# Kernel tuning notes

Measured on AMD Instinct MI355X. Metric: run time of the kernel, lower is better.

## Reference

```python
import jax, jax.numpy as jnp
import numpy as np

B, D, E, H, A = 4096, 1024, 8, 1024, 512  # batch, state_dim, num_options, num_neurons, num_actions


def setup_inputs() -> dict:
    key = jax.random.key(0)
    ks = jax.random.split(key, 16)
    s = 0.02
    return {
        "state": jax.random.normal(ks[0], (B, D), jnp.float32),
        "selected_options": jax.random.randint(ks[1], (B,), 0, E, jnp.int32),
        # option network: Linear(D,H) -> ReLU -> Linear(H,E)
        "Wo1": jax.random.normal(ks[2], (D, H), jnp.float32) * s,
        "bo1": jnp.zeros((H,), jnp.float32),
        "Wo2": jax.random.normal(ks[3], (H, E), jnp.float32) * s,
        "bo2": jnp.zeros((E,), jnp.float32),
        # E expert nets, each: Linear(D,H)+ReLU -> Linear(H,H)+ReLU -> Linear(H,A)
        "We1": jax.random.normal(ks[4], (E, D, H), jnp.float32) * s,
        "be1": jnp.zeros((E, H), jnp.float32),
        "We2": jax.random.normal(ks[5], (E, H, H), jnp.float32) * s,
        "be2": jnp.zeros((E, H), jnp.float32),
        "We3": jax.random.normal(ks[6], (E, H, A), jnp.float32) * s,
        "be3": jnp.zeros((E, A), jnp.float32),
        # termination network: Linear(D,H) -> ReLU -> Linear(H,1) -> Sigmoid
        "Wt1": jax.random.normal(ks[7], (D, H), jnp.float32) * s,
        "bt1": jnp.zeros((H,), jnp.float32),
        "Wt2": jax.random.normal(ks[8], (H, 1), jnp.float32) * s,
        "bt2": jnp.zeros((1,), jnp.float32),
    }


def reference(state, selected_options, Wo1, bo1, Wo2, bo2,
              We1, be1, We2, be2, We3, be3, Wt1, bt1, Wt2, bt2):
    # option head
    option_probs = jax.nn.softmax(jnp.maximum(state @ Wo1 + bo1, 0.0) @ Wo2 + bo2, axis=-1)

    # expert MLPs: compute all experts vectorized, then gather per-sample selected expert.
    # (the torch code loops per sample; equal action sizes so no padding is needed)
    h = jnp.maximum(jnp.einsum("bd,edh->beh", state, We1) + be1, 0.0)   # [B,E,H]
    h = jnp.maximum(jnp.einsum("beh,ehk->bek", h, We2) + be2, 0.0)      # [B,E,H]
    logits = jnp.einsum("beh,eha->bea", h, We3) + be3                   # [B,E,A]
    probs_all = jax.nn.softmax(logits, axis=-1)
    sel = selected_options[:, None, None]
    action_probs = jnp.take_along_axis(probs_all, sel, axis=1)[:, 0, :]  # [B,A]
    selected_actions = jnp.argmax(action_probs, axis=-1)

    # termination head
    termination_prob = jax.nn.sigmoid(jnp.maximum(state @ Wt1 + bt1, 0.0) @ Wt2 + bt2)

    return option_probs, action_probs, termination_prob, selected_options, selected_actions
```

## Files before the change

kernel.cpp:

```cpp
#include <hip/hip_runtime.h>
#include <hip/hip_bf16.h>

#define B_ 4096
#define D_ 1024
#define E_ 8
#define H_ 1024
#define A_ 512
#define PB 6144
#define NTT 24
#define FB_CAP 128
#define FROWS (E_ * FB_CAP)
#define KSPLIT 4
#define MARGIN 3.0e-3f

typedef __attribute__((ext_vector_type(8))) short s16x8;
typedef __attribute__((ext_vector_type(4))) float f32x4;

__device__ __forceinline__ unsigned short f2bf(float f) {
    __hip_bfloat16 h = __float2bfloat16(f);
    return *reinterpret_cast<unsigned short*>(&h);
}
__device__ __forceinline__ float bf2f(unsigned short u) {
    return __uint_as_float(((unsigned int)u) << 16);
}
__device__ __forceinline__ void gload16(const void* g, void* l) {
    __builtin_amdgcn_global_load_lds(
        (const __attribute__((address_space(1))) unsigned int*)g,
        (__attribute__((address_space(3))) unsigned int*)l, 16, 0, 0);
}

__device__ __forceinline__ int a_src_chunk(int lane) { return (((lane & 7) ^ (lane >> 3)) * 8); }

__device__ __forceinline__ int trc(int r, int c) { return (c + r + (r >> 2)) & 63; }

__device__ __forceinline__ void tr_tile_256(const float* __restrict__ src, int Nsrc,
                                            unsigned short* __restrict__ dst, float* T) {
    const int t = threadIdx.x;
    const int c4 = (t & 15) * 4, r0 = t >> 4;
#pragma unroll
    for (int i = 0; i < 8; ++i) {
        const int r = r0 + i * 16;
        const float4 v = *(const float4*)&src[(size_t)r * Nsrc + c4];
        float* Tr = T + r * 64;
        Tr[trc(r, c4 + 0)] = v.x; Tr[trc(r, c4 + 1)] = v.y;
        Tr[trc(r, c4 + 2)] = v.z; Tr[trc(r, c4 + 3)] = v.w;
    }
    __syncthreads();
    const int k4 = (t & 31) * 4, n0 = t >> 5;
#pragma unroll
    for (int i = 0; i < 8; ++i) {
        const int n = n0 + i * 8;
        ushort4 o;
        o.x = f2bf(T[(k4 + 0) * 64 + trc(k4 + 0, n)]);
        o.y = f2bf(T[(k4 + 1) * 64 + trc(k4 + 1, n)]);
        o.z = f2bf(T[(k4 + 2) * 64 + trc(k4 + 2, n)]);
        o.w = f2bf(T[(k4 + 3) * 64 + trc(k4 + 3, n)]);
        *(ushort4*)&dst[(size_t)n * 1024 + k4] = o;
    }
}

__global__ void k_prep(const float* __restrict__ x, unsigned short* __restrict__ y,
                       const float* __restrict__ Wo1, const float* __restrict__ Wt1,
                       unsigned short* __restrict__ Wbf,
                       const float* __restrict__ We1, unsigned short* __restrict__ We1t,
                       const float* __restrict__ We2, unsigned short* __restrict__ We2t,
                       const float* __restrict__ We3, unsigned short* __restrict__ We3t,
                       const int* __restrict__ sel, int* __restrict__ tile_expert,
                       int* __restrict__ rowlist, int* __restrict__ pos_of_row,
                       int* __restrict__ rowlist2, int* __restrict__ cur2) {
    __shared__ float T[128 * 64];
    const int t = threadIdx.x;
    const int bid = blockIdx.x;
    if (bid >= 6401) {
        const int q = bid - 6401;
        const int e = q >> 6, r = q & 63, kt = r >> 3, ntb = r & 7;
        tr_tile_256(We3 + (size_t)e * 524288 + (size_t)(kt * 128) * 512 + ntb * 64, 512,
                    We3t + (size_t)e * 524288 + (size_t)(ntb * 64) * 1024 + kt * 128, T);
        return;
    }
    if (bid >= 5377) {
        const int q = bid - 5377;
        const int e = q >> 7, r = q & 127, kt = r >> 4, ntb = r & 15;
        tr_tile_256(We2 + (size_t)e * 1048576 + (size_t)(kt * 128) * 1024 + ntb * 64, 1024,
                    We2t + (size_t)e * 1048576 + (size_t)(ntb * 64) * 1024 + kt * 128, T);
        return;
    }
    if (bid >= 4353) {
        const int q = bid - 4353;
        const int e = q >> 7, r = q & 127, kt = r >> 4, ntb = r & 15;
        tr_tile_256(We1 + (size_t)e * 1048576 + (size_t)(kt * 128) * 1024 + ntb * 64, 1024,
                    We1t + (size_t)e * 1048576 + (size_t)(ntb * 64) * 1024 + kt * 128, T);
        return;
    }
    if (bid >= 4097) {
        const int q = bid - 4097;
        const int m = q >> 7, r = q & 127, kt = r >> 4, ntb = r & 15;
        const float* src = (m ? Wt1 : Wo1) + (size_t)(kt * 128) * 1024 + ntb * 64;
        tr_tile_256(src, 1024, Wbf + (size_t)(m * 1024 + ntb * 64) * 1024 + kt * 128, T);
        return;
    }
    if (bid > 0) {
        int i = (bid - 1) * 256 + t;
        float4 v = ((const float4*)x)[i];
        ushort4 o;
        o.x = f2bf(v.x); o.y = f2bf(v.y); o.z = f2bf(v.z); o.w = f2bf(v.w);
        ((ushort4*)y)[i] = o;
        return;
    }
    __shared__ int scnt[E_], soff[E_], scur[E_];
    if (t < E_) { scnt[t] = 0; scur[t] = 0; cur2[t] = 0; }
    for (int i = t; i < PB; i += 256) rowlist[i] = -1;
    for (int i = t; i < FROWS; i += 256) rowlist2[i] = -1;
    __syncthreads();
    for (int b = t; b < B_; b += 256) {
        int e = sel[b]; e = e < 0 ? 0 : (e >= E_ ? E_ - 1 : e);
        atomicAdd(&scnt[e], 1);
    }
    __syncthreads();
    if (t == 0) {
        int off = 0;
        for (int e = 0; e < E_; ++e) {
            soff[e] = off;
            int tiles = (scnt[e] + 255) >> 8;
            for (int k = 0; k < tiles; ++k) tile_expert[(off >> 8) + k] = e;
            off += tiles << 8;
        }
        for (int k = off >> 8; k < NTT; ++k) tile_expert[k] = -1;
    }
    __syncthreads();
    for (int b = t; b < B_; b += 256) {
        int e = sel[b]; e = e < 0 ? 0 : (e >= E_ ? E_ - 1 : e);
        int pos = atomicAdd(&scur[e], 1);
        int p = soff[e] + pos; if (p >= PB) p = PB - 1;
        rowlist[p] = b;
        pos_of_row[b] = p;
    }
}

template<int TN>
__device__ __forceinline__ void gemm3(
    const unsigned short* __restrict__ g0, const unsigned short* __restrict__ g1,
    const unsigned short* __restrict__ g2, const unsigned short* __restrict__ g3,
    const unsigned short* __restrict__ Bt, int Kg, const float* __restrict__ bp,
    unsigned short* __restrict__ Cbf, float* __restrict__ Cf, int Ncols, int relu,
    unsigned short* As, unsigned short* Bs)
{
    constexpr int NI = TN / 32;
    constexpr int BTH = TN * 64;
    constexpr int BR = TN / 64;
    const int t = threadIdx.x, lane = t & 63, w = t >> 6;
    const int wr = w >> 1, wc = w & 1;
    const int aseg = w * 2048 + lane * 8;
    const int bseg = w * (BR * 512) + lane * 8;
    const int coffb = a_src_chunk(lane);
    const unsigned short* bsrc = Bt + (size_t)(w * BR * 8 + (lane >> 3)) * Kg + coffb;

    f32x4 acc[4][NI];
#pragma unroll
    for (int i = 0; i < 4; ++i)
#pragma unroll
        for (int j = 0; j < NI; ++j)
#pragma unroll
            for (int r = 0; r < 4; ++r) acc[i][j][r] = 0.f;

#define G_STAGE(IT, BUF) {                                                   \
        const int ko_ = (IT) * 64;                                           \
        const int oa_ = (BUF) * 16384 + aseg;                                \
        gload16(g0 + ko_, As + oa_);                                         \
        gload16(g1 + ko_, As + oa_ + 512);                                   \
        gload16(g2 + ko_, As + oa_ + 1024);                                  \
        gload16(g3 + ko_, As + oa_ + 1536);                                  \
        const int ob_ = (BUF) * BTH + bseg;                                  \
        _Pragma("unroll")                                                    \
        for (int j_ = 0; j_ < BR; ++j_)                                      \
            gload16(bsrc + ko_ + (size_t)(j_ * 8) * Kg, Bs + ob_ + j_ * 512); \
    }

    G_STAGE(0, 0);
    __syncthreads();

    for (int it = 0; it < 16; ++it) {
        const int cb = it & 1;
        if (it + 1 < 16) G_STAGE(it + 1, cb ^ 1);
        __builtin_amdgcn_s_setprio(1);
#pragma unroll
        for (int kq = 0; kq < 2; ++kq) {
            const int sc = kq * 4 + (lane >> 4);
            s16x8 af[4], bfr[NI];
#pragma unroll
            for (int mi = 0; mi < 4; ++mi) {
                const int ar = wr * 64 + mi * 16 + (lane & 15);
                af[mi] = *reinterpret_cast<const s16x8*>(
                    &As[cb * 16384 + ar * 64 + ((sc ^ (ar & 7)) << 3)]);
            }
#pragma unroll
            for (int ni = 0; ni < NI; ++ni) {
                const int br = wc * (TN / 2) + ni * 16 + (lane & 15);
                bfr[ni] = *reinterpret_cast<const s16x8*>(
                    &Bs[cb * BTH + br * 64 + ((sc ^ (br & 7)) << 3)]);
            }
#pragma unroll
            for (int mi = 0; mi < 4; ++mi)
#pragma unroll
                for (int ni = 0; ni < NI; ++ni)
                    acc[mi][ni] = __builtin_amdgcn_mfma_f32_16x16x32_bf16(
                        af[mi], bfr[ni], acc[mi][ni], 0, 0, 0);
        }
        __builtin_amdgcn_s_setprio(0);
        if (it + 1 < 16) __syncthreads();
    }
#undef G_STAGE

    const int cq = lane >> 4, cr = lane & 15;
#pragma unroll
    for (int ni = 0; ni < NI; ++ni) {
        const int col_l = wc * (TN / 2) + ni * 16 + cr;
        const float bv = bp[col_l];
#pragma unroll
        for (int mi = 0; mi < 4; ++mi) {
#pragma unroll
            for (int r = 0; r < 4; ++r) {
                const int row_l = wr * 64 + mi * 16 + cq * 4 + r;
                float v = acc[mi][ni][r] + bv;
                if (relu) v = fmaxf(v, 0.f);
                const size_t idx = (size_t)row_l * Ncols + col_l;
                if (Cbf) Cbf[idx] = f2bf(v);
                if (Cf)  Cf[idx] = v;
            }
        }
    }
}

__global__ __launch_bounds__(512, 2)
void k_d2(const unsigned short* __restrict__ Sbf,
          const int* __restrict__ rowlist, const int* __restrict__ tile_expert,
          const unsigned short* __restrict__ Wbf,
          const float* __restrict__ bo1, const float* __restrict__ bt1,
          const unsigned short* __restrict__ We1t, const float* __restrict__ be1,
          unsigned short* __restrict__ hopt, unsigned short* __restrict__ hterm,
          unsigned short* __restrict__ h1) {
    __shared__ __align__(16) unsigned short SMEM[4 * 16384];
    unsigned short* As = SMEM;
    unsigned short* Bs = SMEM + 2 * 16384;
    const int bid = blockIdx.x;
    const int t = threadIdx.x, lane = t & 63, w = t >> 6;
    const int coff = a_src_chunk(lane);
    const int r0l = w * 32 + (lane >> 3);
    if (bid < 128) {
        const int nt = bid & 7, mt = bid >> 3;
        const unsigned short* g0 = Sbf + (size_t)(mt * 256 + r0l) * D_ + coff;
        const unsigned short* g1 = g0 + (size_t)8 * D_;
        const unsigned short* g2 = g0 + (size_t)16 * D_;
        const unsigned short* g3 = g0 + (size_t)24 * D_;
        int ntRow; const float* bp; unsigned short* C;
        if (nt < 4) { ntRow = nt * 256; bp = bo1 + nt * 256;
                      C = hopt + (size_t)(mt * 256) * H_ + nt * 256; }
        else { ntRow = 1024 + (nt - 4) * 256; bp = bt1 + (nt - 4) * 256;
               C = hterm + (size_t)(mt * 256) * H_ + (nt - 4) * 256; }
        gemm3<256>(g0, g1, g2, g3, Wbf + (size_t)ntRow * 1024, 1024, bp,
                   C, nullptr, H_, 1, As, Bs);
    } else {
        const int q = bid - 128, nt = q & 3, mt = q >> 2;
        const int e = tile_expert[mt]; if (e < 0) return;
        const int base = mt * 256;
        const int sub = rowlist[base]; if (sub < 0) return;
        int r0 = rowlist[base + r0l];      if (r0 < 0) r0 = sub;
        int r1 = rowlist[base + r0l + 8];  if (r1 < 0) r1 = sub;
        int r2 = rowlist[base + r0l + 16]; if (r2 < 0) r2 = sub;
        int r3 = rowlist[base + r0l + 24]; if (r3 < 0) r3 = sub;
        const unsigned short* g0 = Sbf + (size_t)r0 * D_ + coff;
        const unsigned short* g1 = Sbf + (size_t)r1 * D_ + coff;
        const unsigned short* g2 = Sbf + (size_t)r2 * D_ + coff;
        const unsigned short* g3 = Sbf + (size_t)r3 * D_ + coff;
        gemm3<256>(g0, g1, g2, g3,
                   We1t + (size_t)e * 1048576 + (size_t)(nt * 256) * 1024, 1024,
                   be1 + (size_t)e * H_ + nt * 256,
                   h1 + (size_t)(mt * 256) * H_ + nt * 256, nullptr, H_, 1, As, Bs);
    }
}

__global__ __launch_bounds__(512, 2)
void k_d3(const unsigned short* __restrict__ h1, const int* __restrict__ tile_expert,
          const unsigned short* __restrict__ We2t, const float* __restrict__ be2,
          unsigned short* __restrict__ h2) {
    __shared__ __align__(16) unsigned short SMEM[2 * 16384 + 2 * 8192];
    unsigned short* As = SMEM;
    unsigned short* Bs = SMEM + 2 * 16384;
    const int t = threadIdx.x, lane = t & 63, w = t >> 6;
    const int coff = a_src_chunk(lane);
    const int r0l = w * 32 + (lane >> 3);
    const int nt = blockIdx.x & 7, mt = blockIdx.x >> 3;
    const int e = tile_expert[mt]; if (e < 0) return;
    const unsigned short* g0 = h1 + (size_t)(mt * 256 + r0l) * H_ + coff;
    gemm3<128>(g0, g0 + (size_t)8 * H_, g0 + (size_t)16 * H_, g0 + (size_t)24 * H_,
               We2t + (size_t)e * 1048576 + (size_t)(nt * 128) * 1024, 1024,
               be2 + (size_t)e * H_ + nt * 128,
               h2 + (size_t)(mt * 256) * H_ + nt * 128, nullptr, H_, 1, As, Bs);
}

__global__ __launch_bounds__(512, 2)
void k_d5(const unsigned short* __restrict__ h2, const int* __restrict__ tile_expert,
          const unsigned short* __restrict__ We3t, const float* __restrict__ be3,
          float* __restrict__ lgt) {
    __shared__ __align__(16) unsigned short SMEM[2 * 16384 + 2 * 4096];
    unsigned short* As = SMEM;
    unsigned short* Bs = SMEM + 2 * 16384;
    const int t = threadIdx.x, lane = t & 63, w = t >> 6;
    const int coff = a_src_chunk(lane);
    const int r0l = w * 32 + (lane >> 3);
    const int nt = blockIdx.x & 7, mt = blockIdx.x >> 3;
    const int e = tile_expert[mt]; if (e < 0) return;
    const unsigned short* g0 = h2 + (size_t)(mt * 256 + r0l) * H_ + coff;
    gemm3<64>(g0, g0 + (size_t)8 * H_, g0 + (size_t)16 * H_, g0 + (size_t)24 * H_,
              We3t + (size_t)e * 524288 + (size_t)(nt * 64) * 1024, 1024,
              be3 + (size_t)e * A_ + nt * 64,
              nullptr, lgt + (size_t)(mt * 256) * A_ + nt * 64, A_, 0, As, Bs);
}

__device__ __forceinline__ void opt_body(int b, const unsigned short* __restrict__ h,
                                         const float* __restrict__ Wo2, const float* __restrict__ bo2,
                                         float* __restrict__ out, float* sm) {
    const int t = threadIdx.x;
    float acc[E_];
#pragma unroll
    for (int j = 0; j < E_; ++j) acc[j] = 0.f;
    for (int k = t; k < H_; k += 256) {
        float hv = bf2f(h[(size_t)b * H_ + k]);
#pragma unroll
        for (int j = 0; j < E_; ++j) acc[j] = fmaf(hv, Wo2[k * E_ + j], acc[j]);
    }
#pragma unroll
    for (int j = 0; j < E_; ++j)
        for (int off = 32; off; off >>= 1) acc[j] += __shfl_down(acc[j], off, 64);
    float* red = sm;
    float* probs = sm + 4 * E_;
    int wave = t >> 6, lane = t & 63;
    if (lane == 0)
        for (int j = 0; j < E_; ++j) red[wave * E_ + j] = acc[j];
    __syncthreads();
    if (t == 0) {
        float z[E_]; float m = -1e30f;
        for (int j = 0; j < E_; ++j) {
            z[j] = red[j] + red[E_ + j] + red[2 * E_ + j] + red[3 * E_ + j] + bo2[j];
            m = fmaxf(m, z[j]);
        }
        float s = 0.f;
        for (int j = 0; j < E_; ++j) { z[j] = expf(z[j] - m); s += z[j]; }
        float inv = 1.f / s;
        for (int j = 0; j < E_; ++j) probs[j] = z[j] * inv;
    }
    __syncthreads();
    if (t < E_) out[(size_t)b * E_ + t] = probs[t];
}

__device__ __forceinline__ void term_body(int b, const unsigned short* __restrict__ h,
                                          const float* __restrict__ Wt2, const float* __restrict__ bt2,
                                          float* __restrict__ out, float* sm) {
    const int t = threadIdx.x;
    float acc = 0.f;
    for (int k = t; k < H_; k += 256) acc = fmaf(bf2f(h[(size_t)b * H_ + k]), Wt2[k], acc);
    for (int off = 32; off; off >>= 1) acc += __shfl_down(acc, off, 64);
    if ((t & 63) == 0) sm[t >> 6] = acc;
    __syncthreads();
    if (t == 0) {
        float z = sm[0] + sm[1] + sm[2] + sm[3] + bt2[0];
        out[b] = 1.f / (1.f + expf(-z));
    }
}

__global__ __launch_bounds__(256)
void k_gather(const float* __restrict__ logits, const int* __restrict__ pos_of_row,
              const int* __restrict__ sel,
              float* __restrict__ out_probs, float* __restrict__ out_selopt,
              float* __restrict__ out_selact,
              int* __restrict__ rowlist2, int* __restrict__ cur2,
              const unsigned short* __restrict__ hopt, const float* __restrict__ Wo2,
              const float* __restrict__ bo2, float* __restrict__ out_opt,
              const unsigned short* __restrict__ hterm, const float* __restrict__ Wt2,
              const float* __restrict__ bt2, float* __restrict__ out_term) {
    __shared__ float smbuf[5 * E_ + 8];
    const int bid = blockIdx.x;
    if (bid >= 2 * B_) { term_body(bid - 2 * B_, hterm, Wt2, bt2, out_term, smbuf); return; }
    if (bid >= B_)     { opt_body(bid - B_, hopt, Wo2, bo2, out_opt, smbuf); return; }

    const int b = bid;
    int p = pos_of_row[b];
    if (p < 0) p = 0; if (p >= PB) p = PB - 1;
    const int t = threadIdx.x;
    const float* L = logits + (size_t)p * A_;
    float v0 = L[t], v1 = L[t + 256];

    float bv; int bi;
    if (v0 >= v1) { bv = v0; bi = t; } else { bv = v1; bi = t + 256; }
    for (int off = 32; off; off >>= 1) {
        float ov = __shfl_down(bv, off, 64);
        int   oi = __shfl_down(bi, off, 64);
        if (ov > bv || (ov == bv && oi < bi)) { bv = ov; bi = oi; }
    }
    __shared__ float rv[4]; __shared__ int ri[4];
    int wave = t >> 6, lane = t & 63;
    if (lane == 0) { rv[wave] = bv; ri[wave] = bi; }
    __syncthreads();
    __shared__ float sM; __shared__ int sBi;
    if (t == 0) {
        float mv = rv[0]; int mi = ri[0];
        for (int w = 1; w < 4; ++w)
            if (rv[w] > mv || (rv[w] == mv && ri[w] < mi)) { mv = rv[w]; mi = ri[w]; }
        sM = mv; sBi = mi;
    }
    __syncthreads();
    const float M = sM; const int BI = sBi;

    float e0 = expf(v0 - M), e1 = expf(v1 - M);
    float s = e0 + e1;
    for (int off = 32; off; off >>= 1) s += __shfl_down(s, off, 64);
    __shared__ float reds[4];
    if (lane == 0) reds[wave] = s;
    __syncthreads();
    float inv = 1.f / (reds[0] + reds[1] + reds[2] + reds[3]);

    out_probs[(size_t)b * A_ + t]       = e0 * inv;
    out_probs[(size_t)b * A_ + t + 256] = e1 * inv;

    float s0 = (t == BI) ? -1e30f : v0;
    float s1 = (t + 256 == BI) ? -1e30f : v1;
    float sm = fmaxf(s0, s1);
    for (int off = 32; off; off >>= 1) sm = fmaxf(sm, __shfl_down(sm, off, 64));
    __shared__ float red2[4];
    if (lane == 0) red2[wave] = sm;
    __syncthreads();

    if (t == 0) {
        float second = fmaxf(fmaxf(red2[0], red2[1]), fmaxf(red2[2], red2[3]));
        out_selact[b] = (float)BI;
        int e = sel[b]; e = e < 0 ? 0 : (e >= E_ ? E_ - 1 : e);
        out_selopt[b] = (float)sel[b];
        if (M - second < MARGIN) {
            int pos = atomicAdd(&cur2[e], 1);
            if (pos < FB_CAP) rowlist2[e * FB_CAP + pos] = b;
        }
    }
}

#define BM 64
#define BN 64
#define BK 32

__global__ __launch_bounds__(256)
void k_pgemm(const float* __restrict__ A, int lda, const int* __restrict__ flags,
             int gather, const float* __restrict__ W,
             float* __restrict__ P, int K, int N) {
    __shared__ float As_[BK][BM + 4];
    __shared__ float Bs_[BK][BN];

    const int mt = blockIdx.y, nt = blockIdx.x, kz = blockIdx.z;
    if (flags[mt * BM] < 0) return;
    const int e = mt >> 1;
    const float* Wb = W + (size_t)e * K * N + (size_t)nt * BN;

    const int t  = threadIdx.x;
    const int tx = t & 15;
    const int ty = t >> 4;

    const int arow = t >> 3;
    const int ak   = (t & 7) * 4;
    int r0 = mt * BM + arow, r1 = r0 + 32;
    if (gather) { r0 = flags[r0]; r1 = flags[r1]; }
    const int bkr = t >> 4;
    const int bn  = (t & 15) * 4;

    float acc[4][4];
#pragma unroll
    for (int i = 0; i < 4; ++i)
#pragma unroll
        for (int j = 0; j < 4; ++j) acc[i][j] = 0.0f;

    const int kbeg = kz * (K / KSPLIT);
    const int kend = kbeg + (K / KSPLIT);
    for (int k0 = kbeg; k0 < kend; k0 += BK) {
        float4 a0 = make_float4(0.f, 0.f, 0.f, 0.f), a1 = a0;
        if (r0 >= 0) a0 = *(const float4*)&A[(size_t)r0 * lda + k0 + ak];
        if (r1 >= 0) a1 = *(const float4*)&A[(size_t)r1 * lda + k0 + ak];
        float4 b0 = *(const float4*)&Wb[(size_t)(k0 + bkr) * N + bn];
        float4 b1 = *(const float4*)&Wb[(size_t)(k0 + bkr + 16) * N + bn];

        __syncthreads();
        As_[ak + 0][arow] = a0.x; As_[ak + 1][arow] = a0.y;
        As_[ak + 2][arow] = a0.z; As_[ak + 3][arow] = a0.w;
        As_[ak + 0][arow + 32] = a1.x; As_[ak + 1][arow + 32] = a1.y;
        As_[ak + 2][arow + 32] = a1.z; As_[ak + 3][arow + 32] = a1.w;
        *(float4*)&Bs_[bkr][bn]      = b0;
        *(float4*)&Bs_[bkr + 16][bn] = b1;
        __syncthreads();

#pragma unroll
        for (int kk = 0; kk < BK; ++kk) {
            const float4 av = *(const float4*)&As_[kk][ty * 4];
            const float4 bv = *(const float4*)&Bs_[kk][tx * 4];
            const float a_[4] = {av.x, av.y, av.z, av.w};
            const float b_[4] = {bv.x, bv.y, bv.z, bv.w};
#pragma unroll
            for (int i = 0; i < 4; ++i)
#pragma unroll
                for (int j = 0; j < 4; ++j)
                    acc[i][j] = fmaf(a_[i], b_[j], acc[i][j]);
        }
    }

    float* Pz = P + (size_t)kz * FROWS * N;
    const int n0 = nt * BN + tx * 4;
#pragma unroll
    for (int i = 0; i < 4; ++i) {
        int m = mt * BM + ty * 4 + i;
        *(float4*)&Pz[(size_t)m * N + n0] = make_float4(acc[i][0], acc[i][1], acc[i][2], acc[i][3]);
    }
}

__global__ __launch_bounds__(256)
void k_fred(const float* __restrict__ P, const int* __restrict__ flags,
            const float* __restrict__ bias, float* __restrict__ C, int N, int relu) {
    const int m = blockIdx.x;
    if (flags[m] < 0) return;
    const int e = m >> 7;
    const int t = threadIdx.x;
    if (t * 4 >= N) return;
    const size_t MN = (size_t)FROWS * N;
    const size_t base = (size_t)m * N + t * 4;
    float4 s = *(const float4*)&P[base];
#pragma unroll
    for (int z = 1; z < KSPLIT; ++z) {
        float4 p = *(const float4*)&P[(size_t)z * MN + base];
        s.x += p.x; s.y += p.y; s.z += p.z; s.w += p.w;
    }
    const float* bp = bias + (size_t)e * N + t * 4;
    s.x += bp[0]; s.y += bp[1]; s.z += bp[2]; s.w += bp[3];
    if (relu) {
        s.x = fmaxf(s.x, 0.f); s.y = fmaxf(s.y, 0.f);
        s.z = fmaxf(s.z, 0.f); s.w = fmaxf(s.w, 0.f);
    }
    *(float4*)&C[base] = s;
}

__global__ __launch_bounds__(256)
void k_fixup(const float* __restrict__ logitsf, const int* __restrict__ rowlist2,
             float* __restrict__ out_probs, float* __restrict__ out_selact) {
    const int i = blockIdx.x;
    const int row = rowlist2[i];
    if (row < 0) return;
    const int t = threadIdx.x;
    const float* L = logitsf + (size_t)i * A_;
    float v0 = L[t], v1 = L[t + 256];

    float bv; int bi;
    if (v0 >= v1) { bv = v0; bi = t; } else { bv = v1; bi = t + 256; }
    for (int off = 32; off; off >>= 1) {
        float ov = __shfl_down(bv, off, 64);
        int   oi = __shfl_down(bi, off, 64);
        if (ov > bv || (ov == bv && oi < bi)) { bv = ov; bi = oi; }
    }
    __shared__ float rv[4]; __shared__ int ri[4];
    int wave = t >> 6, lane = t & 63;
    if (lane == 0) { rv[wave] = bv; ri[wave] = bi; }
    __syncthreads();
    __shared__ float sM; __shared__ int sBi;
    if (t == 0) {
        float mv = rv[0]; int mi = ri[0];
        for (int w = 1; w < 4; ++w)
            if (rv[w] > mv || (rv[w] == mv && ri[w] < mi)) { mv = rv[w]; mi = ri[w]; }
        sM = mv; sBi = mi;
    }
    __syncthreads();

    float e0 = expf(v0 - sM), e1 = expf(v1 - sM);
    float s = e0 + e1;
    for (int off = 32; off; off >>= 1) s += __shfl_down(s, off, 64);
    __shared__ float reds[4];
    if (lane == 0) reds[wave] = s;
    __syncthreads();
    float inv = 1.f / (reds[0] + reds[1] + reds[2] + reds[3]);

    out_probs[(size_t)row * A_ + t]       = e0 * inv;
    out_probs[(size_t)row * A_ + t + 256] = e1 * inv;
    if (t == 0) out_selact[row] = (float)sBi;
}

extern "C" void kernel_launch(void* const* d_in, const int* in_sizes, int n_in,
                              void* d_out, int out_size, void* d_ws, size_t ws_size,
                              hipStream_t stream) {
    const float* state = (const float*)d_in[0];
    const int*   sel   = (const int*)d_in[1];
    const float* Wo1 = (const float*)d_in[2];
    const float* bo1 = (const float*)d_in[3];
    const float* Wo2 = (const float*)d_in[4];
    const float* bo2 = (const float*)d_in[5];
    const float* We1 = (const float*)d_in[6];
    const float* be1 = (const float*)d_in[7];
    const float* We2 = (const float*)d_in[8];
    const float* be2 = (const float*)d_in[9];
    const float* We3 = (const float*)d_in[10];
    const float* be3 = (const float*)d_in[11];
    const float* Wt1 = (const float*)d_in[12];
    const float* bt1 = (const float*)d_in[13];
    const float* Wt2 = (const float*)d_in[14];
    const float* bt2 = (const float*)d_in[15];
    float* out = (float*)d_out;

    char* w = (char*)d_ws;
    int* meta        = (int*)w;
    int* rowlist     = meta;
    int* pos_of_row  = meta + 6144;
    int* rowlist2    = meta + 10240;
    int* tile_expert = meta + 11264;
    int* cur2        = meta + 11296;
    char* P0 = w + 65536;
    char* P1 = P0 + 12582912;
    char* P2 = P1 + 16777216;
    char* W1 = P2 + 12582912;
    char* W2 = W1 + 16777216;
    char* W3 = W2 + 16777216;
    unsigned short* Sbf   = (unsigned short*)P0;
    unsigned short* Wbf   = (unsigned short*)(P0 + (8u << 20));
    unsigned short* h2b   = (unsigned short*)P0;
    unsigned short* hopt  = (unsigned short*)P1;
    unsigned short* hterm = hopt + (size_t)B_ * H_;
    unsigned short* h1b   = (unsigned short*)P2;
    unsigned short* We1t  = (unsigned short*)W1;
    unsigned short* We2t  = (unsigned short*)W2;
    unsigned short* We3t  = (unsigned short*)W3;
    float* lgt  = (float*)P2;
    float* Pbuf = (float*)P1;
    float* h1f  = (float*)P0;
    float* h2f  = h1f + (size_t)FROWS * H_;
    float* lgf  = h2f + (size_t)FROWS * H_;

    size_t act_off    = (size_t)B_ * E_;
    size_t term_off   = act_off + (size_t)B_ * A_;
    size_t selopt_off = term_off + B_;
    size_t selact_off = selopt_off + B_;

    k_prep<<<6913, 256, 0, stream>>>(state, Sbf, Wo1, Wt1, Wbf, We1, We1t,
                                     We2, We2t, We3, We3t,
                                     sel, tile_expert, rowlist, pos_of_row, rowlist2, cur2);

    k_d2<<<224, 512, 0, stream>>>(Sbf, rowlist, tile_expert, Wbf,
                                  bo1, bt1, We1t, be1, hopt, hterm, h1b);
    k_d3<<<192, 512, 0, stream>>>(h1b, tile_expert, We2t, be2, h2b);
    k_d5<<<192, 512, 0, stream>>>(h2b, tile_expert, We3t, be3, lgt);

    k_gather<<<3 * B_, 256, 0, stream>>>(lgt, pos_of_row, sel,
                                         out + act_off, out + selopt_off, out + selact_off,
                                         rowlist2, cur2,
                                         hopt, Wo2, bo2, out,
                                         hterm, Wt2, bt2, out + term_off);

    k_pgemm<<<dim3(H_ / BN, FROWS / BM, KSPLIT), 256, 0, stream>>>(state, D_, rowlist2, 1, We1, Pbuf, D_, H_);
    k_fred<<<FROWS, 256, 0, stream>>>(Pbuf, rowlist2, be1, h1f, H_, 1);
    k_pgemm<<<dim3(H_ / BN, FROWS / BM, KSPLIT), 256, 0, stream>>>(h1f, H_, rowlist2, 0, We2, Pbuf, H_, H_);
    k_fred<<<FROWS, 256, 0, stream>>>(Pbuf, rowlist2, be2, h2f, H_, 1);
    k_pgemm<<<dim3(A_ / BN, FROWS / BM, KSPLIT), 256, 0, stream>>>(h2f, H_, rowlist2, 0, We3, Pbuf, H_, A_);
    k_fred<<<FROWS, 256, 0, stream>>>(Pbuf, rowlist2, be3, lgf, A_, 0);
    k_fixup<<<FROWS, 256, 0, stream>>>(lgf, rowlist2, out + act_off, out + selact_off);
}
```

Measured before the change: 211.4 us.

## Shrink fallback GEMM row tile and cut prep grid with smaller transpose tiles

The fp32 fallback GEMM row tile drops from 64 to 16 rows, so blocks whose first gathered row is -1 skip work at a finer grain. Each thread now computes one row by four columns instead of a 4x4 tile. The prep kernel transposes in 64x64 halves with a smaller shared buffer and converts four float4s per thread, which roughly halves the block count. In exchange, each fallback block reuses the weight tile across fewer rows, so arithmetic per loaded weight is lower for fully populated tiles.

```diff
diff --git a/kernel.cpp b/kernel.cpp
--- a/kernel.cpp
+++ b/kernel.cpp
@@ -33,12 +33,12 @@
 
 __device__ __forceinline__ int trc(int r, int c) { return (c + r + (r >> 2)) & 63; }
 
-__device__ __forceinline__ void tr_tile_256(const float* __restrict__ src, int Nsrc,
-                                            unsigned short* __restrict__ dst, float* T) {
+__device__ __forceinline__ void tr_tile_64(const float* __restrict__ src, int Nsrc,
+                                           unsigned short* __restrict__ dst, float* T) {
     const int t = threadIdx.x;
     const int c4 = (t & 15) * 4, r0 = t >> 4;
 #pragma unroll
-    for (int i = 0; i < 8; ++i) {
+    for (int i = 0; i < 4; ++i) {
         const int r = r0 + i * 16;
         const float4 v = *(const float4*)&src[(size_t)r * Nsrc + c4];
         float* Tr = T + r * 64;
@@ -46,10 +46,10 @@
         Tr[trc(r, c4 + 2)] = v.z; Tr[trc(r, c4 + 3)] = v.w;
     }
     __syncthreads();
-    const int k4 = (t & 31) * 4, n0 = t >> 5;
-#pragma unroll
-    for (int i = 0; i < 8; ++i) {
-        const int n = n0 + i * 8;
+    const int k4 = (t & 15) * 4, n0 = t >> 4;
+#pragma unroll
+    for (int i = 0; i < 4; ++i) {
+        const int n = n0 + i * 16;
         ushort4 o;
         o.x = f2bf(T[(k4 + 0) * 64 + trc(k4 + 0, n)]);
         o.y = f2bf(T[(k4 + 1) * 64 + trc(k4 + 1, n)]);
@@ -59,52 +59,64 @@
     }
 }
 
-__global__ void k_prep(const float* __restrict__ x, unsigned short* __restrict__ y,
-                       const float* __restrict__ Wo1, const float* __restrict__ Wt1,
-                       unsigned short* __restrict__ Wbf,
-                       const float* __restrict__ We1, unsigned short* __restrict__ We1t,
-                       const float* __restrict__ We2, unsigned short* __restrict__ We2t,
-                       const float* __restrict__ We3, unsigned short* __restrict__ We3t,
-                       const int* __restrict__ sel, int* __restrict__ tile_expert,
-                       int* __restrict__ rowlist, int* __restrict__ pos_of_row,
-                       int* __restrict__ rowlist2, int* __restrict__ cur2) {
-    __shared__ float T[128 * 64];
+__device__ __forceinline__ void tr_tile_128(const float* __restrict__ src, int Nsrc,
+                                            unsigned short* __restrict__ dst, float* T) {
+    tr_tile_64(src, Nsrc, dst, T);
+    __syncthreads();
+    tr_tile_64(src + (size_t)64 * Nsrc, Nsrc, dst + 64, T);
+}
+
+__global__ __launch_bounds__(256)
+void k_prep(const float* __restrict__ x, unsigned short* __restrict__ y,
+            const float* __restrict__ Wo1, const float* __restrict__ Wt1,
+            unsigned short* __restrict__ Wbf,
+            const float* __restrict__ We1, unsigned short* __restrict__ We1t,
+            const float* __restrict__ We2, unsigned short* __restrict__ We2t,
+            const float* __restrict__ We3, unsigned short* __restrict__ We3t,
+            const int* __restrict__ sel, int* __restrict__ tile_expert,
+            int* __restrict__ rowlist, int* __restrict__ pos_of_row,
+            int* __restrict__ rowlist2, int* __restrict__ cur2) {
+    __shared__ float T[64 * 64];
     const int t = threadIdx.x;
     const int bid = blockIdx.x;
-    if (bid >= 6401) {
-        const int q = bid - 6401;
+    if (bid >= 3329) {
+        const int q = bid - 3329;
         const int e = q >> 6, r = q & 63, kt = r >> 3, ntb = r & 7;
-        tr_tile_256(We3 + (size_t)e * 524288 + (size_t)(kt * 128) * 512 + ntb * 64, 512,
+        tr_tile_128(We3 + (size_t)e * 524288 + (size_t)(kt * 128) * 512 + ntb * 64, 512,
                     We3t + (size_t)e * 524288 + (size_t)(ntb * 64) * 1024 + kt * 128, T);
         return;
     }
-    if (bid >= 5377) {
-        const int q = bid - 5377;
+    if (bid >= 2305) {
+        const int q = bid - 2305;
         const int e = q >> 7, r = q & 127, kt = r >> 4, ntb = r & 15;
-        tr_tile_256(We2 + (size_t)e * 1048576 + (size_t)(kt * 128) * 1024 + ntb * 64, 1024,
+        tr_tile_128(We2 + (size_t)e * 1048576 + (size_t)(kt * 128) * 1024 + ntb * 64, 1024,
                     We2t + (size_t)e * 1048576 + (size_t)(ntb * 64) * 1024 + kt * 128, T);
         return;
     }
-    if (bid >= 4353) {
-        const int q = bid - 4353;
+    if (bid >= 1281) {
+        const int q = bid - 1281;
         const int e = q >> 7, r = q & 127, kt = r >> 4, ntb = r & 15;
-        tr_tile_256(We1 + (size_t)e * 1048576 + (size_t)(kt * 128) * 1024 + ntb * 64, 1024,
+        tr_tile_128(We1 + (size_t)e * 1048576 + (size_t)(kt * 128) * 1024 + ntb * 64, 1024,
                     We1t + (size_t)e * 1048576 + (size_t)(ntb * 64) * 1024 + kt * 128, T);
         return;
     }
-    if (bid >= 4097) {
-        const int q = bid - 4097;
+    if (bid >= 1025) {
+        const int q = bid - 1025;
         const int m = q >> 7, r = q & 127, kt = r >> 4, ntb = r & 15;
         const float* src = (m ? Wt1 : Wo1) + (size_t)(kt * 128) * 1024 + ntb * 64;
-        tr_tile_256(src, 1024, Wbf + (size_t)(m * 1024 + ntb * 64) * 1024 + kt * 128, T);
+        tr_tile_128(src, 1024, Wbf + (size_t)(m * 1024 + ntb * 64) * 1024 + kt * 128, T);
         return;
     }
     if (bid > 0) {
-        int i = (bid - 1) * 256 + t;
-        float4 v = ((const float4*)x)[i];
-        ushort4 o;
-        o.x = f2bf(v.x); o.y = f2bf(v.y); o.z = f2bf(v.z); o.w = f2bf(v.w);
-        ((ushort4*)y)[i] = o;
+        const int base = (bid - 1) * 1024 + t;
+#pragma unroll
+        for (int j = 0; j < 4; ++j) {
+            const int i = base + j * 256;
+            float4 v = ((const float4*)x)[i];
+            ushort4 o;
+            o.x = f2bf(v.x); o.y = f2bf(v.y); o.z = f2bf(v.z); o.w = f2bf(v.w);
+            ((ushort4*)y)[i] = o;
+        }
         return;
     }
     __shared__ int scnt[E_], soff[E_], scur[E_];
@@ -442,7 +454,7 @@
     }
 }
 
-#define BM 64
+#define BM 16
 #define BN 64
 #define BK 32
 
@@ -450,70 +462,55 @@
 void k_pgemm(const float* __restrict__ A, int lda, const int* __restrict__ flags,
              int gather, const float* __restrict__ W,
              float* __restrict__ P, int K, int N) {
-    __shared__ float As_[BK][BM + 4];
+    __shared__ float As_[BK][BM + 1];
     __shared__ float Bs_[BK][BN];
 
     const int mt = blockIdx.y, nt = blockIdx.x, kz = blockIdx.z;
     if (flags[mt * BM] < 0) return;
-    const int e = mt >> 1;
+    const int e = mt >> 3;
     const float* Wb = W + (size_t)e * K * N + (size_t)nt * BN;
 
     const int t  = threadIdx.x;
-    const int tx = t & 15;
-    const int ty = t >> 4;
-
-    const int arow = t >> 3;
-    const int ak   = (t & 7) * 4;
-    int r0 = mt * BM + arow, r1 = r0 + 32;
-    if (gather) { r0 = flags[r0]; r1 = flags[r1]; }
+    const int arow = t & 15;
+    const int ak   = ((t >> 4) & 7) * 4;
+    int r0 = mt * BM + arow;
+    if (gather) r0 = flags[r0];
     const int bkr = t >> 4;
     const int bn  = (t & 15) * 4;
-
-    float acc[4][4];
-#pragma unroll
-    for (int i = 0; i < 4; ++i)
-#pragma unroll
-        for (int j = 0; j < 4; ++j) acc[i][j] = 0.0f;
+    const int orow = t >> 4;
+    const int oc4  = (t & 15) * 4;
+
+    float acc[4] = {0.f, 0.f, 0.f, 0.f};
 
     const int kbeg = kz * (K / KSPLIT);
     const int kend = kbeg + (K / KSPLIT);
     for (int k0 = kbeg; k0 < kend; k0 += BK) {
-        float4 a0 = make_float4(0.f, 0.f, 0.f, 0.f), a1 = a0;
-        if (r0 >= 0) a0 = *(const float4*)&A[(size_t)r0 * lda + k0 + ak];
-        if (r1 >= 0) a1 = *(const float4*)&A[(size_t)r1 * lda + k0 + ak];
+        float4 a0 = make_float4(0.f, 0.f, 0.f, 0.f);
+        if (t < 128 && r0 >= 0) a0 = *(const float4*)&A[(size_t)r0 * lda + k0 + ak];
         float4 b0 = *(const float4*)&Wb[(size_t)(k0 + bkr) * N + bn];
         float4 b1 = *(const float4*)&Wb[(size_t)(k0 + bkr + 16) * N + bn];
 
         __syncthreads();
-        As_[ak + 0][arow] = a0.x; As_[ak + 1][arow] = a0.y;
-        As_[ak + 2][arow] = a0.z; As_[ak + 3][arow] = a0.w;
-        As_[ak + 0][arow + 32] = a1.x; As_[ak + 1][arow + 32] = a1.y;
-        As_[ak + 2][arow + 32] = a1.z; As_[ak + 3][arow + 32] = a1.w;
+        if (t < 128) {
+            As_[ak + 0][arow] = a0.x; As_[ak + 1][arow] = a0.y;
+            As_[ak + 2][arow] = a0.z; As_[ak + 3][arow] = a0.w;
+        }
         *(float4*)&Bs_[bkr][bn]      = b0;
         *(float4*)&Bs_[bkr + 16][bn] = b1;
         __syncthreads();
 
 #pragma unroll
         for (int kk = 0; kk < BK; ++kk) {
-            const float4 av = *(const float4*)&As_[kk][ty * 4];
-            const float4 bv = *(const float4*)&Bs_[kk][tx * 4];
-            const float a_[4] = {av.x, av.y, av.z, av.w};
-            const float b_[4] = {bv.x, bv.y, bv.z, bv.w};
-#pragma unroll
-            for (int i = 0; i < 4; ++i)
-#pragma unroll
-                for (int j = 0; j < 4; ++j)
-                    acc[i][j] = fmaf(a_[i], b_[j], acc[i][j]);
+            const float a = As_[kk][orow];
+            const float4 bv = *(const float4*)&Bs_[kk][oc4];
+            acc[0] = fmaf(a, bv.x, acc[0]); acc[1] = fmaf(a, bv.y, acc[1]);
+            acc[2] = fmaf(a, bv.z, acc[2]); acc[3] = fmaf(a, bv.w, acc[3]);
         }
     }
 
     float* Pz = P + (size_t)kz * FROWS * N;
-    const int n0 = nt * BN + tx * 4;
-#pragma unroll
-    for (int i = 0; i < 4; ++i) {
-        int m = mt * BM + ty * 4 + i;
-        *(float4*)&Pz[(size_t)m * N + n0] = make_float4(acc[i][0], acc[i][1], acc[i][2], acc[i][3]);
-    }
+    const int m = mt * BM + orow;
+    *(float4*)&Pz[(size_t)m * N + nt * BN + oc4] = make_float4(acc[0], acc[1], acc[2], acc[3]);
 }
 
 __global__ __launch_bounds__(256)
@@ -638,7 +635,7 @@
     size_t selopt_off = term_off + B_;
     size_t selact_off = selopt_off + B_;
 
-    k_prep<<<6913, 256, 0, stream>>>(state, Sbf, Wo1, Wt1, Wbf, We1, We1t,
+    k_prep<<<3841, 256, 0, stream>>>(state, Sbf, Wo1, Wt1, Wbf, We1, We1t,
                                      We2, We2t, We3, We3t,
                                      sel, tile_expert, rowlist, pos_of_row, rowlist2, cur2);
 
```

Measured after the change: 225.0 us. 1.06x slower.

## Defer We2/We3 weight transposes into the preceding GEMM kernels

Applied to the files above, without the earlier changes.

Moves the fp32-to-bf16 transposes of We2 and We3 out of the prep kernel and into the tails of k_d2 and k_d3. Each block does its GEMM tile and then transposes a few 128x128 weight tiles through shared memory, using a new packed-bf16 transposer with a skewed layout. The aim is to use the idle or tail time of the GEMM grids and shrink the prep launch. We3t now reuses the We1t buffer after layer 1 is done, which saves workspace but depends on strict kernel ordering. Blocks that skip their GEMM now stay alive for the transpose work, and the transpose adds to the GEMM kernels' critical path.

```diff
diff --git a/kernel.cpp b/kernel.cpp
--- a/kernel.cpp
+++ b/kernel.cpp
@@ -59,32 +59,55 @@
     }
 }
 
+__device__ __forceinline__ int t32idx(int k, int c2) {
+    return k * 64 + ((c2 + 5 * (k >> 3) + k) & 63);
+}
+__device__ __forceinline__ void tr_tile_128x128_w512(const float* __restrict__ src, int Nsrc,
+                                                     unsigned short* __restrict__ dst,
+                                                     unsigned int* T32) {
+    const int t = threadIdx.x;
+#pragma unroll
+    for (int i = 0; i < 8; ++i) {
+        const int id = t + i * 512;
+        const int r  = id >> 5;
+        const int c4 = (id & 31) * 4;
+        const float4 v = *(const float4*)&src[(size_t)r * Nsrc + c4];
+        const unsigned int u0 = (unsigned)f2bf(v.x) | ((unsigned)f2bf(v.y) << 16);
+        const unsigned int u1 = (unsigned)f2bf(v.z) | ((unsigned)f2bf(v.w) << 16);
+        T32[t32idx(r, (c4 >> 1) + 0)] = u0;
+        T32[t32idx(r, (c4 >> 1) + 1)] = u1;
+    }
+    __syncthreads();
+#pragma unroll
+    for (int q = 0; q < 4; ++q) {
+        const int id = t + q * 512;
+        const int n = id >> 4;
+        const int L = id & 15;
+        const int hi = n & 1;
+        unsigned int w[4];
+#pragma unroll
+        for (int jj = 0; jj < 4; ++jj) {
+            const int k0 = L * 8 + 2 * jj;
+            const unsigned int a = T32[t32idx(k0,     n >> 1)];
+            const unsigned int b = T32[t32idx(k0 + 1, n >> 1)];
+            const unsigned int ha = hi ? (a >> 16) : (a & 0xffffu);
+            const unsigned int hb = hi ? (b >> 16) : (b & 0xffffu);
+            w[jj] = ha | (hb << 16);
+        }
+        *(uint4*)&dst[(size_t)n * 1024 + L * 8] = make_uint4(w[0], w[1], w[2], w[3]);
+    }
+}
+
 __global__ void k_prep(const float* __restrict__ x, unsigned short* __restrict__ y,
                        const float* __restrict__ Wo1, const float* __restrict__ Wt1,
                        unsigned short* __restrict__ Wbf,
                        const float* __restrict__ We1, unsigned short* __restrict__ We1t,
-                       const float* __restrict__ We2, unsigned short* __restrict__ We2t,
-                       const float* __restrict__ We3, unsigned short* __restrict__ We3t,
                        const int* __restrict__ sel, int* __restrict__ tile_expert,
                        int* __restrict__ rowlist, int* __restrict__ pos_of_row,
                        int* __restrict__ rowlist2, int* __restrict__ cur2) {
     __shared__ float T[128 * 64];
     const int t = threadIdx.x;
     const int bid = blockIdx.x;
-    if (bid >= 6401) {
-        const int q = bid - 6401;
-        const int e = q >> 6, r = q & 63, kt = r >> 3, ntb = r & 7;
-        tr_tile_256(We3 + (size_t)e * 524288 + (size_t)(kt * 128) * 512 + ntb * 64, 512,
-                    We3t + (size_t)e * 524288 + (size_t)(ntb * 64) * 1024 + kt * 128, T);
-        return;
-    }
-    if (bid >= 5377) {
-        const int q = bid - 5377;
-        const int e = q >> 7, r = q & 127, kt = r >> 4, ntb = r & 15;
-        tr_tile_256(We2 + (size_t)e * 1048576 + (size_t)(kt * 128) * 1024 + ntb * 64, 1024,
-                    We2t + (size_t)e * 1048576 + (size_t)(ntb * 64) * 1024 + kt * 128, T);
-        return;
-    }
     if (bid >= 4353) {
         const int q = bid - 4353;
         const int e = q >> 7, r = q & 127, kt = r >> 4, ntb = r & 15;
@@ -237,6 +260,7 @@
           const unsigned short* __restrict__ Wbf,
           const float* __restrict__ bo1, const float* __restrict__ bt1,
           const unsigned short* __restrict__ We1t, const float* __restrict__ be1,
+          const float* __restrict__ We2, unsigned short* __restrict__ We2t,
           unsigned short* __restrict__ hopt, unsigned short* __restrict__ hterm,
           unsigned short* __restrict__ h1) {
     __shared__ __align__(16) unsigned short SMEM[4 * 16384];
@@ -246,6 +270,7 @@
     const int t = threadIdx.x, lane = t & 63, w = t >> 6;
     const int coff = a_src_chunk(lane);
     const int r0l = w * 32 + (lane >> 3);
+
     if (bid < 128) {
         const int nt = bid & 7, mt = bid >> 3;
         const unsigned short* g0 = Sbf + (size_t)(mt * 256 + r0l) * D_ + coff;
@@ -261,41 +286,68 @@
                    C, nullptr, H_, 1, As, Bs);
     } else {
         const int q = bid - 128, nt = q & 3, mt = q >> 2;
-        const int e = tile_expert[mt]; if (e < 0) return;
-        const int base = mt * 256;
-        const int sub = rowlist[base]; if (sub < 0) return;
-        int r0 = rowlist[base + r0l];      if (r0 < 0) r0 = sub;
-        int r1 = rowlist[base + r0l + 8];  if (r1 < 0) r1 = sub;
-        int r2 = rowlist[base + r0l + 16]; if (r2 < 0) r2 = sub;
-        int r3 = rowlist[base + r0l + 24]; if (r3 < 0) r3 = sub;
-        const unsigned short* g0 = Sbf + (size_t)r0 * D_ + coff;
-        const unsigned short* g1 = Sbf + (size_t)r1 * D_ + coff;
-        const unsigned short* g2 = Sbf + (size_t)r2 * D_ + coff;
-        const unsigned short* g3 = Sbf + (size_t)r3 * D_ + coff;
-        gemm3<256>(g0, g1, g2, g3,
-                   We1t + (size_t)e * 1048576 + (size_t)(nt * 256) * 1024, 1024,
-                   be1 + (size_t)e * H_ + nt * 256,
-                   h1 + (size_t)(mt * 256) * H_ + nt * 256, nullptr, H_, 1, As, Bs);
+        const int e = tile_expert[mt];
+        if (e >= 0) {
+            const int base = mt * 256;
+            const int sub = rowlist[base];
+            if (sub >= 0) {
+                int r0 = rowlist[base + r0l];      if (r0 < 0) r0 = sub;
+                int r1 = rowlist[base + r0l + 8];  if (r1 < 0) r1 = sub;
+                int r2 = rowlist[base + r0l + 16]; if (r2 < 0) r2 = sub;
+                int r3 = rowlist[base + r0l + 24]; if (r3 < 0) r3 = sub;
+                const unsigned short* g0 = Sbf + (size_t)r0 * D_ + coff;
+                const unsigned short* g1 = Sbf + (size_t)r1 * D_ + coff;
+                const unsigned short* g2 = Sbf + (size_t)r2 * D_ + coff;
+                const unsigned short* g3 = Sbf + (size_t)r3 * D_ + coff;
+                gemm3<256>(g0, g1, g2, g3,
+                           We1t + (size_t)e * 1048576 + (size_t)(nt * 256) * 1024, 1024,
+                           be1 + (size_t)e * H_ + nt * 256,
+                           h1 + (size_t)(mt * 256) * H_ + nt * 256, nullptr, H_, 1, As, Bs);
+            }
+        }
+    }
+
+    for (int q = bid; q < 512; q += 224) {
+        __syncthreads();
+        const int e = q >> 6, r = q & 63, kt = r >> 3, ntb = r & 7;
+        tr_tile_128x128_w512(We2 + (size_t)e * 1048576 + (size_t)(kt * 128) * 1024 + ntb * 128, 1024,
+                             We2t + (size_t)e * 1048576 + (size_t)(ntb * 128) * 1024 + kt * 128,
+                             (unsigned int*)SMEM);
     }
 }
 
 __global__ __launch_bounds__(512, 2)
 void k_d3(const unsigned short* __restrict__ h1, const int* __restrict__ tile_expert,
           const unsigned short* __restrict__ We2t, const float* __restrict__ be2,
+          const float* __restrict__ We3, unsigned short* __restrict__ We3t,
           unsigned short* __restrict__ h2) {
     __shared__ __align__(16) unsigned short SMEM[2 * 16384 + 2 * 8192];
     unsigned short* As = SMEM;
     unsigned short* Bs = SMEM + 2 * 16384;
+    const int bid = blockIdx.x;
     const int t = threadIdx.x, lane = t & 63, w = t >> 6;
     const int coff = a_src_chunk(lane);
     const int r0l = w * 32 + (lane >> 3);
-    const int nt = blockIdx.x & 7, mt = blockIdx.x >> 3;
-    const int e = tile_expert[mt]; if (e < 0) return;
-    const unsigned short* g0 = h1 + (size_t)(mt * 256 + r0l) * H_ + coff;
-    gemm3<128>(g0, g0 + (size_t)8 * H_, g0 + (size_t)16 * H_, g0 + (size_t)24 * H_,
-               We2t + (size_t)e * 1048576 + (size_t)(nt * 128) * 1024, 1024,
-               be2 + (size_t)e * H_ + nt * 128,
-               h2 + (size_t)(mt * 256) * H_ + nt * 128, nullptr, H_, 1, As, Bs);
+
+    {
+        const int nt = bid & 7, mt = bid >> 3;
+        const int e = tile_expert[mt];
+        if (e >= 0) {
+            const unsigned short* g0 = h1 + (size_t)(mt * 256 + r0l) * H_ + coff;
+            gemm3<128>(g0, g0 + (size_t)8 * H_, g0 + (size_t)16 * H_, g0 + (size_t)24 * H_,
+                       We2t + (size_t)e * 1048576 + (size_t)(nt * 128) * 1024, 1024,
+                       be2 + (size_t)e * H_ + nt * 128,
+                       h2 + (size_t)(mt * 256) * H_ + nt * 128, nullptr, H_, 1, As, Bs);
+        }
+    }
+
+    for (int q = bid; q < 256; q += 192) {
+        __syncthreads();
+        const int e = q >> 5, r = q & 31, kt = r >> 2, ntb = r & 3;
+        tr_tile_128x128_w512(We3 + (size_t)e * 524288 + (size_t)(kt * 128) * 512 + ntb * 128, 512,
+                             We3t + (size_t)e * 524288 + (size_t)(ntb * 128) * 1024 + kt * 128,
+                             (unsigned int*)SMEM);
+    }
 }
 
 __global__ __launch_bounds__(512, 2)
@@ -617,7 +669,6 @@
     char* P2 = P1 + 16777216;
     char* W1 = P2 + 12582912;
     char* W2 = W1 + 16777216;
-    char* W3 = W2 + 16777216;
     unsigned short* Sbf   = (unsigned short*)P0;
     unsigned short* Wbf   = (unsigned short*)(P0 + (8u << 20));
     unsigned short* h2b   = (unsigned short*)P0;
@@ -625,8 +676,8 @@
     unsigned short* hterm = hopt + (size_t)B_ * H_;
     unsigned short* h1b   = (unsigned short*)P2;
     unsigned short* We1t  = (unsigned short*)W1;
+    unsigned short* We3t  = (unsigned short*)W1;
     unsigned short* We2t  = (unsigned short*)W2;
-    unsigned short* We3t  = (unsigned short*)W3;
     float* lgt  = (float*)P2;
     float* Pbuf = (float*)P1;
     float* h1f  = (float*)P0;
@@ -638,13 +689,12 @@
     size_t selopt_off = term_off + B_;
     size_t selact_off = selopt_off + B_;
 
-    k_prep<<<6913, 256, 0, stream>>>(state, Sbf, Wo1, Wt1, Wbf, We1, We1t,
-                                     We2, We2t, We3, We3t,
+    k_prep<<<5377, 256, 0, stream>>>(state, Sbf, Wo1, Wt1, Wbf, We1, We1t,
                                      sel, tile_expert, rowlist, pos_of_row, rowlist2, cur2);
 
     k_d2<<<224, 512, 0, stream>>>(Sbf, rowlist, tile_expert, Wbf,
-                                  bo1, bt1, We1t, be1, hopt, hterm, h1b);
-    k_d3<<<192, 512, 0, stream>>>(h1b, tile_expert, We2t, be2, h2b);
+                                  bo1, bt1, We1t, be1, We2, We2t, hopt, hterm, h1b);
+    k_d3<<<192, 512, 0, stream>>>(h1b, tile_expert, We2t, be2, We3, We3t, h2b);
     k_d5<<<192, 512, 0, stream>>>(h2b, tile_expert, We3t, be3, lgt);
 
     k_gather<<<3 * B_, 256, 0, stream>>>(lgt, pos_of_row, sel,
```

Result: slower. 217.9 us (+3.1%).
